# Performance work log

Measured on AMD Instinct MI355X. Metric: run time of the kernel, lower is better.

## Reference

```python
import jax, jax.numpy as jnp
import numpy as np

B, S, IN, OUT = 4, 8192, 768, 768
ALPHA = 0.01


def setup_inputs() -> dict:
    key = jax.random.key(0)
    kx, kw, kb = jax.random.split(key, 3)
    x = jax.random.randint(kx, (B, S, IN), -127, 127, dtype=jnp.int8)
    weight = jax.random.randint(kw, (IN, OUT), -127, 127, dtype=jnp.int8)
    bias = (jax.random.normal(kb, (1, OUT), dtype=jnp.float32) * 0.1).astype(jnp.float16)
    alpha = jnp.float32(ALPHA)
    return {"x": x, "weight": weight, "bias": bias, "alpha": alpha}


def reference(x, weight, bias, alpha):
    # x: [B, S, IN] int8, weight: [IN, OUT] int8 (Conv1D layout), bias: [1, OUT] fp16
    x_shape = x.shape
    xf = x.reshape(-1, x_shape[-1])                      # [N, IN] int8

    # rand_elements = zeros of x dtype (int8) -> masked_x == x, but keep the
    # wrap-bit detection chain faithful to the source.
    rand_elements = jnp.zeros_like(xf)                   # int8 zeros
    masked_x = xf + rand_elements                        # int8 wraparound add
    m32 = masked_x.astype(jnp.int32)
    x32 = xf.astype(jnp.int32)
    r32 = rand_elements.astype(jnp.int32)
    wraps = ((m32 ^ x32) & (m32 ^ r32) & 128) >> 7       # [N, IN] int32 (all zero here)
    wraps = jnp.where((wraps < 0) & (m32 < 0), 1, wraps)
    wraps = wraps.astype(jnp.int8)

    wf = weight.astype(jnp.float32)                      # [IN, OUT]
    # F.linear(masked_x.float(), weight.t().float()) == masked_x @ weight
    hidden = masked_x.astype(jnp.float32) @ wf           # [N, OUT] fp32
    overflow = ((wraps.astype(jnp.float32) @ wf).astype(jnp.int32) << 8)
    hidden = hidden + overflow.astype(jnp.float32)

    mask_mul = jnp.zeros((xf.shape[0], OUT), dtype=jnp.float32)
    y = hidden - mask_mul
    fp_y = y * alpha + bias.astype(jnp.float32)          # dequant scale + bias
    yq = jnp.clip(jnp.round(fp_y), -128, 127).astype(jnp.int8)
    return yq.reshape(*x_shape[:-1], -1)
```

## Files before the change

### kernel.cpp

```cpp
#include <hip/hip_runtime.h>

#define M_TOT 32768
#define K_TOT 768
#define N_TOT 768

typedef int v4i __attribute__((ext_vector_type(4)));

#define GLOAD_LDS(g, l) __builtin_amdgcn_global_load_lds( \
    (const __attribute__((address_space(1))) unsigned int*)(g), \
    (__attribute__((address_space(3))) unsigned int*)(l), 16, 0, 0)

__device__ __forceinline__ unsigned pack4(v4i a) {
  unsigned lo = __builtin_amdgcn_perm((unsigned)a.y, (unsigned)a.x, 0x00000400u);
  unsigned hi = __builtin_amdgcn_perm((unsigned)a.w, (unsigned)a.z, 0x00000400u);
  return __builtin_amdgcn_perm(hi, lo, 0x05040100u);
}

__global__ __launch_bounds__(256) void pack_w_kernel(const int* __restrict__ W,
                                                     signed char* __restrict__ W8T) {
  __shared__ signed char t[64][72];
  const int k0 = blockIdx.x * 64, n0 = blockIdx.y * 64;
  for (int i = threadIdx.x; i < 4096; i += 256) {
    int k = i >> 6, n = i & 63;
    t[n][k] = (signed char)W[(k0 + k) * N_TOT + n0 + n];
  }
  __syncthreads();
  for (int i = threadIdx.x; i < 4096; i += 256) {
    int n = i >> 6, k = i & 63;
    W8T[(n0 + n) * K_TOT + k0 + k] = t[n][k];
  }
}

__global__ __launch_bounds__(256, 2) void gemm_i8_kernel(
    const int* __restrict__ X, const signed char* __restrict__ W8T,
    const float* __restrict__ bias, const float* __restrict__ alpha_p,
    int* __restrict__ out) {
  __shared__ __align__(16) signed char Abuf[2][8192];
  __shared__ __align__(16) signed char Bbuf[3][8192];

  const int d = blockIdx.x;
  const int t = (d & 7) * 192 + (d >> 3);
  const int mt = t / 6, nt = t - mt * 6;
  const int row0 = mt << 7, col0 = nt << 7;

  const int tid = threadIdx.x;
  const int lane = tid & 63;
  const int wave = tid >> 6;
  const int wr = wave >> 1, wc = wave & 1;
  const int fr = lane & 15, fg = lane >> 4;
  const int fsw = (fr & 3) << 4;

  const int arow = tid >> 4;
  const int acol = (tid & 15) << 2;
  const int* Xbase = X + (row0 + arow) * K_TOT + acol;
  const int awsw = (arow & 3) << 4;

  int bsrc[2], bdst[2];
#pragma unroll
  for (int i = 0; i < 2; ++i) {
    int c = i * 256 + tid;
    int r = c >> 2, s = (c & 3) << 4;
    bsrc[i] = (col0 + r) * K_TOT + (s ^ ((r & 3) << 4));
    bdst[i] = i * 4096 + wave * 1024;
  }

  v4i q[2][8];
  const v4i zero = {0, 0, 0, 0};
  v4i acc[4][4];
#pragma unroll
  for (int m = 0; m < 4; ++m)
#pragma unroll
    for (int n = 0; n < 4; ++n) acc[m][n] = zero;

#define ISSUE_A(ks)                                                      \
  do {                                                                   \
    const int* _p = Xbase + (ks) * 64;                                   \
    _Pragma("unroll") for (int j = 0; j < 8; ++j)                        \
        q[(ks) & 1][j] = *(const v4i*)(_p + j * 16 * K_TOT);             \
  } while (0)

#define ISSUE_B(ks)                                                      \
  do {                                                                   \
    const signed char* _w = W8T + (ks) * 64;                             \
    signed char* _lb = Bbuf[(ks) % 3];                                   \
    GLOAD_LDS(_w + bsrc[0], _lb + bdst[0]);                              \
    GLOAD_LDS(_w + bsrc[1], _lb + bdst[1]);                              \
  } while (0)

#define PACK_WRITE_A(tt)                                                 \
  do {                                                                   \
    signed char* _ab = Abuf[(tt) & 1];                                   \
    _Pragma("unroll") for (int j = 0; j < 8; ++j) {                      \
      unsigned _dw = pack4(q[(tt) & 1][j]);                              \
      *(unsigned*)&_ab[(16 * j + arow) * 64 + (acol ^ awsw)] = _dw;      \
    }                                                                    \
  } while (0)

#define FRAGS_MFMA(ks)                                                   \
  do {                                                                   \
    v4i af[4], bf[4];                                                    \
    const signed char* _ab = Abuf[(ks) & 1];                             \
    const signed char* _bb = Bbuf[(ks) % 3];                             \
    const int _kb = (fg << 4) ^ fsw;                                     \
    _Pragma("unroll") for (int m = 0; m < 4; ++m)                        \
        af[m] = *(const v4i*)&_ab[(wr * 64 + m * 16 + fr) * 64 + _kb];   \
    _Pragma("unroll") for (int n = 0; n < 4; ++n)                        \
        bf[n] = *(const v4i*)&_bb[(wc * 64 + n * 16 + fr) * 64 + _kb];   \
    _Pragma("unroll") for (int m = 0; m < 4; ++m)                        \
        _Pragma("unroll") for (int n = 0; n < 4; ++n)                    \
            acc[m][n] = __builtin_amdgcn_mfma_i32_16x16x64_i8(           \
                af[m], bf[n], acc[m][n], 0, 0, 0);                       \
  } while (0)

#define GITER(ks, TOPW, MIDW)                                            \
  do {                                                                   \
    asm volatile("s_waitcnt vmcnt(" TOPW ") lgkmcnt(0)" ::: "memory");   \
    __builtin_amdgcn_s_barrier();                                        \
    if ((ks) + 2 < 12) { ISSUE_A((ks) + 2); ISSUE_B((ks) + 2); }         \
    FRAGS_MFMA(ks);                                                      \
    if ((ks) + 1 < 12) {                                                 \
      asm volatile("s_waitcnt vmcnt(" MIDW ")" ::: "memory");            \
      PACK_WRITE_A((ks) + 1);                                            \
    }                                                                    \
  } while (0)

  ISSUE_A(0); ISSUE_B(0);
  ISSUE_A(1); ISSUE_B(1);
  asm volatile("s_waitcnt vmcnt(12)" ::: "memory");
  PACK_WRITE_A(0);

  GITER(0, "10", "12");
  GITER(1, "10", "12");
  GITER(2, "10", "12");
  GITER(3, "10", "12");
  GITER(4, "10", "12");
  GITER(5, "10", "12");
  GITER(6, "10", "12");
  GITER(7, "10", "12");
  GITER(8, "10", "12");
  GITER(9, "10", "12");
  GITER(10, "10", "2");
  GITER(11, "0", "0");

  const float alpha = *alpha_p;
  float bv[4];
#pragma unroll
  for (int n = 0; n < 4; ++n) bv[n] = bias[col0 + wc * 64 + n * 16 + fr];

#pragma unroll
  for (int m = 0; m < 4; ++m) {
    int orow = row0 + wr * 64 + m * 16 + fg * 4;
#pragma unroll
    for (int n = 0; n < 4; ++n) {
      int ocol = col0 + wc * 64 + n * 16 + fr;
      int* po = out + orow * N_TOT + ocol;
#pragma unroll
      for (int r = 0; r < 4; ++r) {
        float v = rintf((float)acc[m][n][r] * alpha + bv[n]);
        v = fminf(127.f, fmaxf(-128.f, v));
        po[r * N_TOT] = (int)v;
      }
    }
  }
}

extern "C" void kernel_launch(void* const* d_in, const int* in_sizes, int n_in,
                              void* d_out, int out_size, void* d_ws, size_t ws_size,
                              hipStream_t stream) {
  const int* X = (const int*)d_in[0];
  const int* W = (const int*)d_in[1];
  const float* bias = (const float*)d_in[2];
  const float* alpha = (const float*)d_in[3];
  int* out = (int*)d_out;
  signed char* W8T = (signed char*)d_ws;

  dim3 pg(K_TOT / 64, N_TOT / 64);
  pack_w_kernel<<<pg, 256, 0, stream>>>(W, W8T);
  gemm_i8_kernel<<<(M_TOT / 128) * (N_TOT / 128), 256, 0, stream>>>(X, W8T, bias, alpha, out);
}
```

Before: 55.04 us.

## Pre-pack int32 activations to int8 in a separate pass, DMA both operands to LDS

Adds a pack_x kernel that narrows the int32-stored activations to int8 in workspace. The GEMM then streams both A and B with global_load_lds into triple-buffered LDS, removing register staging and the per-block repacking of A. Occupancy is raised to 3 blocks per CU and MFMA sections get s_setprio. The pack pass adds an extra read of X (about 100MB) plus a 25MB write, but the GEMM no longer re-reads the int32 X for each of the 6 column tiles. The old path is kept as a fallback when the workspace is too small.

```diff
diff --git a/kernel.cpp b/kernel.cpp
--- a/kernel.cpp
+++ b/kernel.cpp
@@ -5,6 +5,7 @@
 #define N_TOT 768
 
 typedef int v4i __attribute__((ext_vector_type(4)));
+typedef unsigned int v4u __attribute__((ext_vector_type(4)));
 
 #define GLOAD_LDS(g, l) __builtin_amdgcn_global_load_lds( \
     (const __attribute__((address_space(1))) unsigned int*)(g), \
@@ -31,12 +32,28 @@
   }
 }
 
-__global__ __launch_bounds__(256, 2) void gemm_i8_kernel(
-    const int* __restrict__ X, const signed char* __restrict__ W8T,
+__global__ __launch_bounds__(256) void pack_x_kernel(const int* __restrict__ X,
+                                                     unsigned* __restrict__ X8) {
+  const int gtid = blockIdx.x * 256 + threadIdx.x;
+  const int NT = 2048 * 256;
+#pragma unroll
+  for (int b = 0; b < 3; ++b) {
+    v4i v[4];
+#pragma unroll
+    for (int j = 0; j < 4; ++j)
+      v[j] = *(const v4i*)(X + (size_t)((b * 4 + j) * NT + gtid) * 4);
+#pragma unroll
+    for (int j = 0; j < 4; ++j)
+      X8[(b * 4 + j) * NT + gtid] = pack4(v[j]);
+  }
+}
+
+__global__ __launch_bounds__(256, 3) void gemm_i8_p2(
+    const signed char* __restrict__ X8, const signed char* __restrict__ W8T,
     const float* __restrict__ bias, const float* __restrict__ alpha_p,
     int* __restrict__ out) {
-  __shared__ __align__(16) signed char Abuf[2][8192];
-  __shared__ __align__(16) signed char Bbuf[3][8192];
+  __shared__ __align__(16) signed char Albuf[3][8192];
+  __shared__ __align__(16) signed char Blbuf[3][8192];
 
   const int d = blockIdx.x;
   const int t = (d & 7) * 192 + (d >> 3);
@@ -50,11 +67,120 @@
   const int fr = lane & 15, fg = lane >> 4;
   const int fsw = (fr & 3) << 4;
 
+  int asrc[2], bsrc[2], sdst[2];
+#pragma unroll
+  for (int i = 0; i < 2; ++i) {
+    int c = i * 256 + tid;
+    int r = c >> 2, s = (c & 3) << 4;
+    int sw = s ^ ((r & 3) << 4);
+    asrc[i] = (row0 + r) * K_TOT + sw;
+    bsrc[i] = (col0 + r) * K_TOT + sw;
+    sdst[i] = i * 4096 + wave * 1024;
+  }
+
+  const v4i zero = {0, 0, 0, 0};
+  v4i acc[4][4];
+#pragma unroll
+  for (int m = 0; m < 4; ++m)
+#pragma unroll
+    for (int n = 0; n < 4; ++n) acc[m][n] = zero;
+
+#define P2_ISSUE(ks)                                                     \
+  do {                                                                   \
+    const signed char* _xa = X8 + (ks) * 64;                             \
+    const signed char* _wb = W8T + (ks) * 64;                            \
+    signed char* _la = Albuf[(ks) % 3];                                  \
+    signed char* _lb = Blbuf[(ks) % 3];                                  \
+    GLOAD_LDS(_xa + asrc[0], _la + sdst[0]);                             \
+    GLOAD_LDS(_xa + asrc[1], _la + sdst[1]);                             \
+    GLOAD_LDS(_wb + bsrc[0], _lb + sdst[0]);                             \
+    GLOAD_LDS(_wb + bsrc[1], _lb + sdst[1]);                             \
+  } while (0)
+
+#define P2_MFMA(ks)                                                      \
+  do {                                                                   \
+    v4i af[4], bf[4];                                                    \
+    const signed char* _ab = Albuf[(ks) % 3];                            \
+    const signed char* _bb = Blbuf[(ks) % 3];                            \
+    const int _kb = (fg << 4) ^ fsw;                                     \
+    _Pragma("unroll") for (int m = 0; m < 4; ++m)                        \
+        af[m] = *(const v4i*)&_ab[(wr * 64 + m * 16 + fr) * 64 + _kb];   \
+    _Pragma("unroll") for (int n = 0; n < 4; ++n)                        \
+        bf[n] = *(const v4i*)&_bb[(wc * 64 + n * 16 + fr) * 64 + _kb];   \
+    __builtin_amdgcn_s_setprio(1);                                       \
+    _Pragma("unroll") for (int m = 0; m < 4; ++m)                        \
+        _Pragma("unroll") for (int n = 0; n < 4; ++n)                    \
+            acc[m][n] = __builtin_amdgcn_mfma_i32_16x16x64_i8(           \
+                af[m], bf[n], acc[m][n], 0, 0, 0);                       \
+    __builtin_amdgcn_s_setprio(0);                                       \
+  } while (0)
+
+#define P2_ITER(ks, TOPW, DOI)                                           \
+  do {                                                                   \
+    asm volatile("s_waitcnt vmcnt(" TOPW ")" ::: "memory");              \
+    __builtin_amdgcn_s_barrier();                                        \
+    if (DOI) P2_ISSUE((ks) + 2);                                         \
+    P2_MFMA(ks);                                                         \
+  } while (0)
+
+  P2_ISSUE(0);
+  P2_ISSUE(1);
+
+  P2_ITER(0, "4", 1);
+  P2_ITER(1, "4", 1);
+  P2_ITER(2, "4", 1);
+  P2_ITER(3, "4", 1);
+  P2_ITER(4, "4", 1);
+  P2_ITER(5, "4", 1);
+  P2_ITER(6, "4", 1);
+  P2_ITER(7, "4", 1);
+  P2_ITER(8, "4", 1);
+  P2_ITER(9, "4", 1);
+  P2_ITER(10, "4", 0);
+  P2_ITER(11, "0", 0);
+
+  const float alpha = *alpha_p;
+  float bv[4];
+#pragma unroll
+  for (int n = 0; n < 4; ++n) bv[n] = bias[col0 + wc * 64 + n * 16 + fr];
+
+#pragma unroll
+  for (int m = 0; m < 4; ++m) {
+    int orow = row0 + wr * 64 + m * 16 + fg * 4;
+#pragma unroll
+    for (int n = 0; n < 4; ++n) {
+      int ocol = col0 + wc * 64 + n * 16 + fr;
+      int* po = out + orow * N_TOT + ocol;
+#pragma unroll
+      for (int r = 0; r < 4; ++r) {
+        float v = rintf((float)acc[m][n][r] * alpha + bv[n]);
+        v = fminf(127.f, fmaxf(-128.f, v));
+        po[r * N_TOT] = (int)v;
+      }
+    }
+  }
+}
+
+__global__ __launch_bounds__(256, 2) void gemm_i8_fb(
+    const int* __restrict__ X, const signed char* __restrict__ W8T,
+    const float* __restrict__ bias, const float* __restrict__ alpha_p,
+    int* __restrict__ out) {
+  __shared__ __align__(16) signed char Abuf[2][8192];
+  __shared__ __align__(16) signed char Bbuf[3][8192];
+  const int d = blockIdx.x;
+  const int t = (d & 7) * 192 + (d >> 3);
+  const int mt = t / 6, nt = t - mt * 6;
+  const int row0 = mt << 7, col0 = nt << 7;
+  const int tid = threadIdx.x;
+  const int lane = tid & 63;
+  const int wave = tid >> 6;
+  const int wr = wave >> 1, wc = wave & 1;
+  const int fr = lane & 15, fg = lane >> 4;
+  const int fsw = (fr & 3) << 4;
   const int arow = tid >> 4;
   const int acol = (tid & 15) << 2;
   const int* Xbase = X + (row0 + arow) * K_TOT + acol;
   const int awsw = (arow & 3) << 4;
-
   int bsrc[2], bdst[2];
 #pragma unroll
   for (int i = 0; i < 2; ++i) {
@@ -63,7 +189,6 @@
     bsrc[i] = (col0 + r) * K_TOT + (s ^ ((r & 3) << 4));
     bdst[i] = i * 4096 + wave * 1024;
   }
-
   v4i q[2][8];
   const v4i zero = {0, 0, 0, 0};
   v4i acc[4][4];
@@ -71,23 +196,20 @@
   for (int m = 0; m < 4; ++m)
 #pragma unroll
     for (int n = 0; n < 4; ++n) acc[m][n] = zero;
-
-#define ISSUE_A(ks)                                                      \
+#define FB_ISSUE_A(ks)                                                   \
   do {                                                                   \
     const int* _p = Xbase + (ks) * 64;                                   \
     _Pragma("unroll") for (int j = 0; j < 8; ++j)                        \
         q[(ks) & 1][j] = *(const v4i*)(_p + j * 16 * K_TOT);             \
   } while (0)
-
-#define ISSUE_B(ks)                                                      \
+#define FB_ISSUE_B(ks)                                                   \
   do {                                                                   \
     const signed char* _w = W8T + (ks) * 64;                             \
     signed char* _lb = Bbuf[(ks) % 3];                                   \
     GLOAD_LDS(_w + bsrc[0], _lb + bdst[0]);                              \
     GLOAD_LDS(_w + bsrc[1], _lb + bdst[1]);                              \
   } while (0)
-
-#define PACK_WRITE_A(tt)                                                 \
+#define FB_PACK_A(tt)                                                    \
   do {                                                                   \
     signed char* _ab = Abuf[(tt) & 1];                                   \
     _Pragma("unroll") for (int j = 0; j < 8; ++j) {                      \
@@ -95,8 +217,7 @@
       *(unsigned*)&_ab[(16 * j + arow) * 64 + (acol ^ awsw)] = _dw;      \
     }                                                                    \
   } while (0)
-
-#define FRAGS_MFMA(ks)                                                   \
+#define FB_MFMA(ks)                                                      \
   do {                                                                   \
     v4i af[4], bf[4];                                                    \
     const signed char* _ab = Abuf[(ks) & 1];                             \
@@ -106,47 +227,44 @@
         af[m] = *(const v4i*)&_ab[(wr * 64 + m * 16 + fr) * 64 + _kb];   \
     _Pragma("unroll") for (int n = 0; n < 4; ++n)                        \
         bf[n] = *(const v4i*)&_bb[(wc * 64 + n * 16 + fr) * 64 + _kb];   \
+    __builtin_amdgcn_s_setprio(1);                                       \
     _Pragma("unroll") for (int m = 0; m < 4; ++m)                        \
         _Pragma("unroll") for (int n = 0; n < 4; ++n)                    \
             acc[m][n] = __builtin_amdgcn_mfma_i32_16x16x64_i8(           \
                 af[m], bf[n], acc[m][n], 0, 0, 0);                       \
-  } while (0)
-
-#define GITER(ks, TOPW, MIDW)                                            \
+    __builtin_amdgcn_s_setprio(0);                                       \
+  } while (0)
+#define FB_ITER(ks, TOPW, MIDW)                                          \
   do {                                                                   \
     asm volatile("s_waitcnt vmcnt(" TOPW ") lgkmcnt(0)" ::: "memory");   \
     __builtin_amdgcn_s_barrier();                                        \
-    if ((ks) + 2 < 12) { ISSUE_A((ks) + 2); ISSUE_B((ks) + 2); }         \
-    FRAGS_MFMA(ks);                                                      \
+    if ((ks) + 2 < 12) { FB_ISSUE_A((ks) + 2); FB_ISSUE_B((ks) + 2); }   \
+    FB_MFMA(ks);                                                         \
     if ((ks) + 1 < 12) {                                                 \
       asm volatile("s_waitcnt vmcnt(" MIDW ")" ::: "memory");            \
-      PACK_WRITE_A((ks) + 1);                                            \
+      FB_PACK_A((ks) + 1);                                               \
     }                                                                    \
   } while (0)
-
-  ISSUE_A(0); ISSUE_B(0);
-  ISSUE_A(1); ISSUE_B(1);
+  FB_ISSUE_A(0); FB_ISSUE_B(0);
+  FB_ISSUE_A(1); FB_ISSUE_B(1);
   asm volatile("s_waitcnt vmcnt(12)" ::: "memory");
-  PACK_WRITE_A(0);
-
-  GITER(0, "10", "12");
-  GITER(1, "10", "12");
-  GITER(2, "10", "12");
-  GITER(3, "10", "12");
-  GITER(4, "10", "12");
-  GITER(5, "10", "12");
-  GITER(6, "10", "12");
-  GITER(7, "10", "12");
-  GITER(8, "10", "12");
-  GITER(9, "10", "12");
-  GITER(10, "10", "2");
-  GITER(11, "0", "0");
-
+  FB_PACK_A(0);
+  FB_ITER(0, "10", "12");
+  FB_ITER(1, "10", "12");
+  FB_ITER(2, "10", "12");
+  FB_ITER(3, "10", "12");
+  FB_ITER(4, "10", "12");
+  FB_ITER(5, "10", "12");
+  FB_ITER(6, "10", "12");
+  FB_ITER(7, "10", "12");
+  FB_ITER(8, "10", "12");
+  FB_ITER(9, "10", "12");
+  FB_ITER(10, "10", "2");
+  FB_ITER(11, "0", "0");
   const float alpha = *alpha_p;
   float bv[4];
 #pragma unroll
   for (int n = 0; n < 4; ++n) bv[n] = bias[col0 + wc * 64 + n * 16 + fr];
-
 #pragma unroll
   for (int m = 0; m < 4; ++m) {
     int orow = row0 + wr * 64 + m * 16 + fg * 4;
@@ -172,9 +290,19 @@
   const float* bias = (const float*)d_in[2];
   const float* alpha = (const float*)d_in[3];
   int* out = (int*)d_out;
+
   signed char* W8T = (signed char*)d_ws;
+  signed char* X8 = (signed char*)d_ws + (1 << 20);
 
   dim3 pg(K_TOT / 64, N_TOT / 64);
   pack_w_kernel<<<pg, 256, 0, stream>>>(W, W8T);
-  gemm_i8_kernel<<<(M_TOT / 128) * (N_TOT / 128), 256, 0, stream>>>(X, W8T, bias, alpha, out);
-}
+
+  if (ws_size >= (size_t)(1 << 20) + (size_t)M_TOT * K_TOT) {
+    pack_x_kernel<<<2048, 256, 0, stream>>>(X, (unsigned*)X8);
+    gemm_i8_p2<<<(M_TOT / 128) * (N_TOT / 128), 256, 0, stream>>>(
+        X8, W8T, bias, alpha, out);
+  } else {
+    gemm_i8_fb<<<(M_TOT / 128) * (N_TOT / 128), 256, 0, stream>>>(
+        X, W8T, bias, alpha, out);
+  }
+}
```

After: 67.88 us. 23.3% more time.
